# Kernel optimization log

Measured on AMD Instinct MI355X. Metric: run time of the kernel, lower is better.

Reference implementation:

```python
import jax, jax.numpy as jnp
import numpy as np

NUM_GROUPS = 32
EPS = 1e-6


def group_norm(x, gamma, beta):
    # x: [B, C, H, W]
    B, C, H, W = x.shape
    xg = x.reshape(B, NUM_GROUPS, C // NUM_GROUPS, H, W)
    mean = jnp.mean(xg, axis=(2, 3, 4), keepdims=True)
    var = jnp.var(xg, axis=(2, 3, 4), keepdims=True)
    xn = ((xg - mean) * jax.lax.rsqrt(var + EPS)).reshape(B, C, H, W)
    return xn * gamma[None, :, None, None] + beta[None, :, None, None]


def conv1x1(x, w, b):
    # x: [B, C, H, W], w: [O, C], b: [O]  (1x1 conv == channel matmul)
    return jnp.einsum('oc,bchw->bohw', w, x) + b[None, :, None, None]


def setup_inputs() -> dict:
    key = jax.random.key(0)
    ks = jax.random.split(key, 10)
    B, C, H, W = 16, 512, 32, 32
    s = 1.0 / np.sqrt(C)
    inp = {
        'hidden_states': jax.random.normal(ks[0], (B, C, H, W), dtype=jnp.float32),
        'norm_gamma': jnp.ones((C,), dtype=jnp.float32),
        'norm_beta': jnp.zeros((C,), dtype=jnp.float32),
        'wq': jax.random.normal(ks[1], (C, C), dtype=jnp.float32) * s,
        'bq': jnp.zeros((C,), dtype=jnp.float32),
        'wk': jax.random.normal(ks[2], (C, C), dtype=jnp.float32) * s,
        'bk': jnp.zeros((C,), dtype=jnp.float32),
        'wv': jax.random.normal(ks[3], (C, C), dtype=jnp.float32) * s,
        'bv': jnp.zeros((C,), dtype=jnp.float32),
        'wo': jax.random.normal(ks[4], (C, C), dtype=jnp.float32) * s,
        'bo': jnp.zeros((C,), dtype=jnp.float32),
    }
    return inp


def reference(hidden_states, norm_gamma, norm_beta, wq, bq, wk, bk, wv, bv, wo, bo):
    residual = hidden_states
    h = group_norm(hidden_states, norm_gamma, norm_beta)
    q = conv1x1(h, wq, bq)  # [B, C, H, W]
    k = conv1x1(h, wk, bk)
    v = conv1x1(h, wv, bv)
    B, C, H, W = q.shape
    N = H * W
    qf = q.reshape(B, C, N)  # [B, C, N]
    kf = k.reshape(B, C, N)
    vf = v.reshape(B, C, N)
    scale = float(C) ** (-0.5)
    # attn_weights[b, i, j] = sum_c q[b,c,i] * k[b,c,j]
    attn = jnp.einsum('bci,bcj->bij', qf, kf) * scale
    attn = jax.nn.softmax(attn, axis=2)
    # out[b, c, i] = sum_j v[b,c,j] * attn[b,i,j]
    out = jnp.einsum('bcj,bij->bci', vf, attn).reshape(B, C, H, W)
    out = conv1x1(out, wo, bo)
    return residual + out
```

## Files before the change

kernel.cpp:

```cpp
#include <hip/hip_runtime.h>

typedef __attribute__((ext_vector_type(4))) float f32x4;
typedef __attribute__((ext_vector_type(8))) __bf16 bf16x8;
typedef __attribute__((ext_vector_type(4))) unsigned short us4;
typedef __attribute__((ext_vector_type(8))) unsigned short us8;

#define B_  16
#define C_  512
#define N_  1024
#define G_  32
#define GS  16

__device__ inline unsigned short f2bf(float f) {
  unsigned u = __builtin_bit_cast(unsigned, f);
  u += 0x7fffu + ((u >> 16) & 1u);
  return (unsigned short)(u >> 16);
}
__device__ inline float bf2f(unsigned short u) {
  unsigned x = (unsigned)u << 16;
  return __builtin_bit_cast(float, x);
}

#define GLOAD_LDS16(gp, lp) __builtin_amdgcn_global_load_lds( \
    (const __attribute__((address_space(1))) unsigned int*)(gp), \
    (__attribute__((address_space(3))) unsigned int*)(lp), 16, 0, 0)

__global__ __launch_bounds__(256) void gn_stats(const float* __restrict__ x,
                                                float* __restrict__ stats) {
  int bg = blockIdx.x;
  const float* xp = x + (long)bg * (GS * N_);
  int tid = threadIdx.x;
  float s = 0.f, ss = 0.f;
  for (int i = tid * 4; i < GS * N_; i += 1024) {
    f32x4 v = *(const f32x4*)&xp[i];
    s += v.x + v.y + v.z + v.w;
    ss += v.x * v.x + v.y * v.y + v.z * v.z + v.w * v.w;
  }
  __shared__ float r1[256], r2[256];
  r1[tid] = s; r2[tid] = ss; __syncthreads();
  for (int off = 128; off > 0; off >>= 1) {
    if (tid < off) { r1[tid] += r1[tid + off]; r2[tid] += r2[tid + off]; }
    __syncthreads();
  }
  if (tid == 0) {
    float mean = r1[0] * (1.f / (GS * N_));
    float var  = r2[0] * (1.f / (GS * N_)) - mean * mean;
    stats[bg * 2]     = mean;
    stats[bg * 2 + 1] = rsqrtf(var + 1e-6f);
  }
}

__global__ __launch_bounds__(256) void gn_apply(const float* __restrict__ x,
                                                const float* __restrict__ stats,
                                                const float* __restrict__ gamma,
                                                const float* __restrict__ beta,
                                                unsigned short* __restrict__ ht) {
  int b = blockIdx.z, ct = blockIdx.y, nt = blockIdx.x;
  int c0 = ct * 64, n0 = nt * 64;
  int tid = threadIdx.x;
  __shared__ unsigned short L[64 * 68];
  const float* xp = x + ((long)b * C_ + c0) * N_ + n0;
#pragma unroll
  for (int i = 0; i < 4; ++i) {
    int li = tid + i * 256;
    int row = li >> 4;
    int col4 = (li & 15) * 4;
    f32x4 v = *(const f32x4*)&xp[(long)row * N_ + col4];
    int c = c0 + row;
    float mean = stats[(b * G_ + (c >> 4)) * 2];
    float rstd = stats[(b * G_ + (c >> 4)) * 2 + 1];
    float gm = gamma[c] * rstd;
    float bt = beta[c] - mean * gm;
    us4 o;
    o.x = f2bf(v.x * gm + bt); o.y = f2bf(v.y * gm + bt);
    o.z = f2bf(v.z * gm + bt); o.w = f2bf(v.w * gm + bt);
    *(us4*)&L[row * 68 + col4] = o;
  }
  __syncthreads();
#pragma unroll
  for (int i = 0; i < 2; ++i) {
    int s = tid + i * 256;
    int n = s >> 3;
    int cs = (s & 7) * 8;
    us8 o;
#pragma unroll
    for (int j = 0; j < 8; ++j) o[j] = L[(cs + j) * 68 + n];
    *(us8*)&ht[((long)b * N_ + n0 + n) * C_ + c0 + cs] = o;
  }
}

__global__ __launch_bounds__(256) void convert_w(const float* __restrict__ wq, const float* __restrict__ wk,
                                                 const float* __restrict__ wv, const float* __restrict__ wo,
                                                 const float* __restrict__ bq, const float* __restrict__ bk,
                                                 unsigned short* __restrict__ wqk, unsigned short* __restrict__ wvb,
                                                 unsigned short* __restrict__ wob, float* __restrict__ bqk) {
  int i = blockIdx.x * 256 + threadIdx.x;
  if (i < C_ * C_) {
    wqk[i]           = f2bf(wq[i]);
    wqk[C_ * C_ + i] = f2bf(wk[i]);
    wvb[i]           = f2bf(wv[i]);
    wob[i]           = f2bf(wo[i]);
  }
  if (i < C_) { bqk[i] = bq[i]; bqk[C_ + i] = bk[i]; }
}

__device__ inline f32x4 mfma16(bf16x8 a, bf16x8 b, f32x4 c) {
  return __builtin_amdgcn_mfma_f32_16x16x32_bf16(a, b, c, 0, 0, 0);
}

template<int EPI>
__global__ __launch_bounds__(256) void gemm_k(
    const unsigned short* __restrict__ A, long lda, long Az,
    const unsigned short* __restrict__ Bm, long ldb, long Bz,
    void* __restrict__ Dp, long ldd, long Dz,
    const float* __restrict__ bias, float scale, int K,
    const float* __restrict__ residual, float* __restrict__ rs) {
  const int z = blockIdx.z;
  const long row0 = (long)blockIdx.x * 128;
  const long col0 = (long)blockIdx.y * 128;
  const int tid  = threadIdx.x;
  const int lane = tid & 63;
  const int wave = tid >> 6;
  const int wr = (wave >> 1) * 64;
  const int wc = (wave & 1) * 64;
  const int lr = lane & 15;
  const int kh = (lane >> 4) * 8;

  __shared__ unsigned short As[2][128 * 32];
  __shared__ unsigned short Bs[2][128 * 32];
  __shared__ float dinv[128];

  if constexpr (EPI == 6) {
    if (tid < 128) {
      const float* rp = rs + ((long)z * 1024 + row0 + tid) * 16;
      float s = 0.f;
#pragma unroll
      for (int i = 0; i < 16; ++i) s += rp[i];
      dinv[tid] = 1.f / s;
    }
  }

  const int sr  = (lane >> 2);
  const int sk  = (lane & 3) * 8;
  const unsigned short* ga0 = A  + (long)z * Az + (row0 + wave * 32 + sr) * lda + sk;
  const unsigned short* gb0 = Bm + (long)z * Bz + (col0 + wave * 32 + sr) * ldb + sk;

  f32x4 acc[4][4];
#pragma unroll
  for (int m = 0; m < 4; ++m)
#pragma unroll
    for (int n = 0; n < 4; ++n) acc[m][n] = f32x4{0.f, 0.f, 0.f, 0.f};

  GLOAD_LDS16(ga0, &As[0][wave * 1024]);
  GLOAD_LDS16(ga0 + 16 * lda, &As[0][wave * 1024 + 512]);
  GLOAD_LDS16(gb0, &Bs[0][wave * 1024]);
  GLOAD_LDS16(gb0 + 16 * ldb, &Bs[0][wave * 1024 + 512]);
  __syncthreads();

  int cur = 0;
  for (int k0 = 0; k0 < K; k0 += 32) {
    if (k0 + 32 < K) {
      const int nb = cur ^ 1;
      GLOAD_LDS16(ga0 + k0 + 32, &As[nb][wave * 1024]);
      GLOAD_LDS16(ga0 + 16 * lda + k0 + 32, &As[nb][wave * 1024 + 512]);
      GLOAD_LDS16(gb0 + k0 + 32, &Bs[nb][wave * 1024]);
      GLOAD_LDS16(gb0 + 16 * ldb + k0 + 32, &Bs[nb][wave * 1024 + 512]);
    }
    bf16x8 af[4], bfr[4];
#pragma unroll
    for (int m = 0; m < 4; ++m) af[m]  = *(const bf16x8*)&As[cur][(wr + m * 16 + lr) * 32 + kh];
#pragma unroll
    for (int n = 0; n < 4; ++n) bfr[n] = *(const bf16x8*)&Bs[cur][(wc + n * 16 + lr) * 32 + kh];
#pragma unroll
    for (int m = 0; m < 4; ++m)
#pragma unroll
      for (int n = 0; n < 4; ++n)
        acc[m][n] = mfma16(af[m], bfr[n], acc[m][n]);
    __syncthreads();
    cur ^= 1;
  }

  const int rb = (lane >> 4) * 4;
  if constexpr (EPI == 5) {
    const int jt = (int)blockIdx.y;
#pragma unroll
    for (int m = 0; m < 4; ++m) {
      float ps[4] = {0.f, 0.f, 0.f, 0.f};
#pragma unroll
      for (int n = 0; n < 4; ++n) {
#pragma unroll
        for (int r = 0; r < 4; ++r) {
          long gr = row0 + wr + m * 16 + rb + r;
          long gc = col0 + wc + n * 16 + lr;
          float e = exp2f(acc[m][n][r] * scale);
          ((unsigned short*)Dp)[(long)z * Dz + gr * ldd + gc] = f2bf(e);
          ps[r] += e;
        }
      }
#pragma unroll
      for (int r = 0; r < 4; ++r) {
#pragma unroll
        for (int off = 1; off < 16; off <<= 1) ps[r] += __shfl_xor(ps[r], off);
      }
      if (lr == 0) {
#pragma unroll
        for (int r = 0; r < 4; ++r) {
          long gr = row0 + wr + m * 16 + rb + r;
          rs[((long)z * 1024 + gr) * 16 + jt * 2 + (wave & 1)] = ps[r];
        }
      }
    }
    return;
  }

#pragma unroll
  for (int m = 0; m < 4; ++m) {
#pragma unroll
    for (int n = 0; n < 4; ++n) {
#pragma unroll
      for (int r = 0; r < 4; ++r) {
        long gr = row0 + wr + m * 16 + rb + r;
        long gc = col0 + wc + n * 16 + lr;
        float v = acc[m][n][r];
        if constexpr (EPI == 0) {
          v += bias[gc];
          ((unsigned short*)Dp)[(long)z * Dz + gr * ldd + gc] = f2bf(v);
        } else if constexpr (EPI == 1) {
          v += bias[gr];
          ((unsigned short*)Dp)[(long)z * Dz + gr * ldd + gc] = f2bf(v);
        } else if constexpr (EPI == 6) {
          v *= dinv[(int)(gr - row0)];
          ((unsigned short*)Dp)[(long)z * Dz + gr * ldd + gc] = f2bf(v);
        } else {
          long o = (long)z * (512L * 1024L) + gr * 1024L + gc;
          ((float*)Dp)[o] = v + bias[gr] + residual[o];
        }
      }
    }
  }
}

extern "C" void kernel_launch(void* const* d_in, const int* in_sizes, int n_in,
                              void* d_out, int out_size, void* d_ws, size_t ws_size,
                              hipStream_t stream) {
  const float* x     = (const float*)d_in[0];
  const float* gamma = (const float*)d_in[1];
  const float* beta  = (const float*)d_in[2];
  const float* wq    = (const float*)d_in[3];
  const float* bq    = (const float*)d_in[4];
  const float* wk    = (const float*)d_in[5];
  const float* bk    = (const float*)d_in[6];
  const float* wv    = (const float*)d_in[7];
  const float* bv    = (const float*)d_in[8];
  const float* wo    = (const float*)d_in[9];
  const float* bo    = (const float*)d_in[10];
  float* out = (float*)d_out;

  char* ws = (char*)d_ws;
  unsigned short* ht   = (unsigned short*)(ws + 0);
  unsigned short* qkt  = (unsigned short*)(ws + 16777216);
  unsigned short* vv   = (unsigned short*)(ws + 50331648);
  unsigned short* ot   = (unsigned short*)(ws + 67108864);
  unsigned short* S    = (unsigned short*)(ws + 83886080);
  unsigned short* wqkb = (unsigned short*)(ws + 117440512);
  unsigned short* wvb  = (unsigned short*)(ws + 119537664);
  unsigned short* wob  = (unsigned short*)(ws + 120061952);
  float* bqk           = (float*)(ws + 120586240);
  float* stats         = (float*)(ws + 120590336);
  float* rs            = (float*)(ws + 120594432);

  convert_w<<<1024, 256, 0, stream>>>(wq, wk, wv, wo, bq, bk, wqkb, wvb, wob, bqk);
  gn_stats<<<512, 256, 0, stream>>>(x, stats);
  gn_apply<<<dim3(16, 8, 16), 256, 0, stream>>>(x, stats, gamma, beta, ht);

  gemm_k<0><<<dim3(128, 8, 1), 256, 0, stream>>>(ht, 512, 0, wqkb, 512, 0,
                                                 qkt, 1024, 0, bqk, 0.f, 512, nullptr, nullptr);
  gemm_k<1><<<dim3(4, 128, 1), 256, 0, stream>>>(wvb, 512, 0, ht, 512, 0,
                                                 vv, 16384, 0, bv, 0.f, 512, nullptr, nullptr);
  gemm_k<5><<<dim3(8, 8, 16), 256, 0, stream>>>(qkt, 1024, 1048576L, qkt + 512, 1024, 1048576L,
                                                S, 1024, 1048576L, nullptr,
                                                0.06375871416f, 512, nullptr, rs);
  gemm_k<6><<<dim3(8, 4, 16), 256, 0, stream>>>(S, 1024, 1048576L,
                                                vv, 16384, 1024,
                                                ot, 512, 524288L, nullptr, 0.f, 1024, nullptr, rs);
  gemm_k<4><<<dim3(4, 8, 16), 256, 0, stream>>>(wob, 512, 0, ot, 512, 524288L,
                                                out, 0, 0, bo, 0.f, 512, x, nullptr);
}
```

Before: 158.7 us.

## Replace 128x128 GEMM with 256-row tiled, swizzled, 512-thread pipelined GEMM

Rewrites the shared bf16 MFMA GEMM to use 256xBN tiles with 8 waves, a K-step of 64, and an XOR-swizzled LDS layout to avoid bank conflicts. It adds manual vmcnt waits and raw barriers so the next tile's loads overlap the MFMA work, and raises MFMA priority with setprio. All five GEMM launches get new grid shapes, and the softmax row-sum partial indexing changes to four partials per column tile. The larger tiles raise data reuse and arithmetic intensity, at the cost of fewer blocks per launch and more register pressure. The prefetch wraps around to tile 0 at the final iteration, which issues a redundant load.

```diff
diff --git a/kernel.cpp b/kernel.cpp
--- a/kernel.cpp
+++ b/kernel.cpp
@@ -15,10 +15,6 @@
   unsigned u = __builtin_bit_cast(unsigned, f);
   u += 0x7fffu + ((u >> 16) & 1u);
   return (unsigned short)(u >> 16);
-}
-__device__ inline float bf2f(unsigned short u) {
-  unsigned x = (unsigned)u << 16;
-  return __builtin_bit_cast(float, x);
 }
 
 #define GLOAD_LDS16(gp, lp) __builtin_amdgcn_global_load_lds( \
@@ -108,90 +104,123 @@
   return __builtin_amdgcn_mfma_f32_16x16x32_bf16(a, b, c, 0, 0, 0);
 }
 
-template<int EPI>
-__global__ __launch_bounds__(256) void gemm_k(
+__device__ inline int swz(int b) { return b ^ (((b >> 9) & 1) << 5); }
+
+template<int NREP, int EPI>
+__global__ __launch_bounds__(512, 2) void gemm256(
     const unsigned short* __restrict__ A, long lda, long Az,
     const unsigned short* __restrict__ Bm, long ldb, long Bz,
     void* __restrict__ Dp, long ldd, long Dz,
     const float* __restrict__ bias, float scale, int K,
     const float* __restrict__ residual, float* __restrict__ rs) {
+  constexpr int BN = NREP * 64;
   const int z = blockIdx.z;
-  const long row0 = (long)blockIdx.x * 128;
-  const long col0 = (long)blockIdx.y * 128;
+  const long row0 = (long)blockIdx.x * 256;
+  const long col0 = (long)blockIdx.y * BN;
   const int tid  = threadIdx.x;
   const int lane = tid & 63;
   const int wave = tid >> 6;
-  const int wr = (wave >> 1) * 64;
-  const int wc = (wave & 1) * 64;
+  const int wm = wave >> 2;
+  const int wn = wave & 3;
   const int lr = lane & 15;
-  const int kh = (lane >> 4) * 8;
-
-  __shared__ unsigned short As[2][128 * 32];
-  __shared__ unsigned short Bs[2][128 * 32];
-  __shared__ float dinv[128];
+  const int khb = (lane >> 4) * 16;
+
+  __shared__ unsigned short Abuf[2][16384];
+  __shared__ unsigned short Bbuf[2][BN * 64];
+  __shared__ float dinv_s[256];
+
+  const unsigned short* Ab = A  + (long)z * Az;
+  const unsigned short* Bb = Bm + (long)z * Bz;
 
   if constexpr (EPI == 6) {
-    if (tid < 128) {
+    if (tid < 256) {
       const float* rp = rs + ((long)z * 1024 + row0 + tid) * 16;
       float s = 0.f;
 #pragma unroll
       for (int i = 0; i < 16; ++i) s += rp[i];
-      dinv[tid] = 1.f / s;
+      dinv_s[tid] = 1.f / s;
     }
-  }
-
-  const int sr  = (lane >> 2);
-  const int sk  = (lane & 3) * 8;
-  const unsigned short* ga0 = A  + (long)z * Az + (row0 + wave * 32 + sr) * lda + sk;
-  const unsigned short* gb0 = Bm + (long)z * Bz + (col0 + wave * 32 + sr) * ldb + sk;
-
-  f32x4 acc[4][4];
-#pragma unroll
-  for (int m = 0; m < 4; ++m)
-#pragma unroll
-    for (int n = 0; n < 4; ++n) acc[m][n] = f32x4{0.f, 0.f, 0.f, 0.f};
-
-  GLOAD_LDS16(ga0, &As[0][wave * 1024]);
-  GLOAD_LDS16(ga0 + 16 * lda, &As[0][wave * 1024 + 512]);
-  GLOAD_LDS16(gb0, &Bs[0][wave * 1024]);
-  GLOAD_LDS16(gb0 + 16 * ldb, &Bs[0][wave * 1024 + 512]);
-  __syncthreads();
-
-  int cur = 0;
-  for (int k0 = 0; k0 < K; k0 += 32) {
-    if (k0 + 32 < K) {
-      const int nb = cur ^ 1;
-      GLOAD_LDS16(ga0 + k0 + 32, &As[nb][wave * 1024]);
-      GLOAD_LDS16(ga0 + 16 * lda + k0 + 32, &As[nb][wave * 1024 + 512]);
-      GLOAD_LDS16(gb0 + k0 + 32, &Bs[nb][wave * 1024]);
-      GLOAD_LDS16(gb0 + 16 * ldb + k0 + 32, &Bs[nb][wave * 1024 + 512]);
+    asm volatile("s_waitcnt lgkmcnt(0)" ::: "memory");
+  }
+
+  const unsigned short* gA[4];
+#pragma unroll
+  for (int r = 0; r < 4; ++r) {
+    int L = swz(r * 8192 + tid * 16);
+    gA[r] = Ab + (row0 + (L >> 7)) * lda + ((L & 127) >> 1);
+  }
+  const unsigned short* gB[NREP];
+#pragma unroll
+  for (int r = 0; r < NREP; ++r) {
+    int L = swz(r * 8192 + tid * 16);
+    gB[r] = Bb + (col0 + (L >> 7)) * ldb + ((L & 127) >> 1);
+  }
+
+  f32x4 acc[8][NREP];
+#pragma unroll
+  for (int m = 0; m < 8; ++m)
+#pragma unroll
+    for (int n = 0; n < NREP; ++n) acc[m][n] = f32x4{0.f, 0.f, 0.f, 0.f};
+
+  const int NT = K >> 6;
+#pragma unroll
+  for (int r = 0; r < 4; ++r)    GLOAD_LDS16(gA[r], &Abuf[0][r * 4096 + wave * 512]);
+#pragma unroll
+  for (int r = 0; r < NREP; ++r) GLOAD_LDS16(gB[r], &Bbuf[0][r * 4096 + wave * 512]);
+
+  for (int t = 0; t < NT; ++t) {
+    int tn = t + 1; if (tn == NT) tn = 0;
+    const long ko = (long)tn << 6;
+    const int nb = (t + 1) & 1;
+#pragma unroll
+    for (int r = 0; r < 4; ++r)    GLOAD_LDS16(gA[r] + ko, &Abuf[nb][r * 4096 + wave * 512]);
+#pragma unroll
+    for (int r = 0; r < NREP; ++r) GLOAD_LDS16(gB[r] + ko, &Bbuf[nb][r * 4096 + wave * 512]);
+    if constexpr (NREP == 4) asm volatile("s_waitcnt vmcnt(8)" ::: "memory");
+    else                     asm volatile("s_waitcnt vmcnt(6)" ::: "memory");
+    __builtin_amdgcn_s_barrier();
+    __builtin_amdgcn_sched_barrier(0);
+    const unsigned short* Al = Abuf[t & 1];
+    const unsigned short* Bl = Bbuf[t & 1];
+#pragma unroll
+    for (int kk = 0; kk < 2; ++kk) {
+      bf16x8 af[8], bfr[NREP];
+#pragma unroll
+      for (int m = 0; m < 8; ++m) {
+        int Pb = swz((wm * 128 + m * 16 + lr) * 128 + kk * 64 + khb);
+        af[m] = *(const bf16x8*)((const char*)Al + Pb);
+      }
+#pragma unroll
+      for (int n = 0; n < NREP; ++n) {
+        int Pb = swz((wn * NREP * 16 + n * 16 + lr) * 128 + kk * 64 + khb);
+        bfr[n] = *(const bf16x8*)((const char*)Bl + Pb);
+      }
+      __builtin_amdgcn_s_setprio(1);
+#pragma unroll
+      for (int m = 0; m < 8; ++m)
+#pragma unroll
+        for (int n = 0; n < NREP; ++n)
+          acc[m][n] = mfma16(af[m], bfr[n], acc[m][n]);
+      __builtin_amdgcn_s_setprio(0);
     }
-    bf16x8 af[4], bfr[4];
-#pragma unroll
-    for (int m = 0; m < 4; ++m) af[m]  = *(const bf16x8*)&As[cur][(wr + m * 16 + lr) * 32 + kh];
-#pragma unroll
-    for (int n = 0; n < 4; ++n) bfr[n] = *(const bf16x8*)&Bs[cur][(wc + n * 16 + lr) * 32 + kh];
-#pragma unroll
-    for (int m = 0; m < 4; ++m)
-#pragma unroll
-      for (int n = 0; n < 4; ++n)
-        acc[m][n] = mfma16(af[m], bfr[n], acc[m][n]);
-    __syncthreads();
-    cur ^= 1;
-  }
+    __builtin_amdgcn_sched_barrier(0);
+    __builtin_amdgcn_s_barrier();
+    __builtin_amdgcn_sched_barrier(0);
+  }
+  asm volatile("s_waitcnt vmcnt(0)" ::: "memory");
 
   const int rb = (lane >> 4) * 4;
   if constexpr (EPI == 5) {
-    const int jt = (int)blockIdx.y;
-#pragma unroll
-    for (int m = 0; m < 4; ++m) {
+    const int jt = blockIdx.y;
+#pragma unroll
+    for (int m = 0; m < 8; ++m) {
       float ps[4] = {0.f, 0.f, 0.f, 0.f};
 #pragma unroll
-      for (int n = 0; n < 4; ++n) {
+      for (int n = 0; n < NREP; ++n) {
 #pragma unroll
         for (int r = 0; r < 4; ++r) {
-          long gr = row0 + wr + m * 16 + rb + r;
-          long gc = col0 + wc + n * 16 + lr;
+          long gr = row0 + wm * 128 + m * 16 + rb + r;
+          long gc = col0 + wn * NREP * 16 + n * 16 + lr;
           float e = exp2f(acc[m][n][r] * scale);
           ((unsigned short*)Dp)[(long)z * Dz + gr * ldd + gc] = f2bf(e);
           ps[r] += e;
@@ -199,14 +228,16 @@
       }
 #pragma unroll
       for (int r = 0; r < 4; ++r) {
-#pragma unroll
-        for (int off = 1; off < 16; off <<= 1) ps[r] += __shfl_xor(ps[r], off);
+        ps[r] += __shfl_xor(ps[r], 1);
+        ps[r] += __shfl_xor(ps[r], 2);
+        ps[r] += __shfl_xor(ps[r], 4);
+        ps[r] += __shfl_xor(ps[r], 8);
       }
       if (lr == 0) {
 #pragma unroll
         for (int r = 0; r < 4; ++r) {
-          long gr = row0 + wr + m * 16 + rb + r;
-          rs[((long)z * 1024 + gr) * 16 + jt * 2 + (wave & 1)] = ps[r];
+          long gr = row0 + wm * 128 + m * 16 + rb + r;
+          rs[((long)z * 1024 + gr) * 16 + jt * 4 + wn] = ps[r];
         }
       }
     }
@@ -214,13 +245,13 @@
   }
 
 #pragma unroll
-  for (int m = 0; m < 4; ++m) {
-#pragma unroll
-    for (int n = 0; n < 4; ++n) {
+  for (int m = 0; m < 8; ++m) {
+#pragma unroll
+    for (int n = 0; n < NREP; ++n) {
 #pragma unroll
       for (int r = 0; r < 4; ++r) {
-        long gr = row0 + wr + m * 16 + rb + r;
-        long gc = col0 + wc + n * 16 + lr;
+        long gr = row0 + wm * 128 + m * 16 + rb + r;
+        long gc = col0 + wn * NREP * 16 + n * 16 + lr;
         float v = acc[m][n][r];
         if constexpr (EPI == 0) {
           v += bias[gc];
@@ -229,7 +260,7 @@
           v += bias[gr];
           ((unsigned short*)Dp)[(long)z * Dz + gr * ldd + gc] = f2bf(v);
         } else if constexpr (EPI == 6) {
-          v *= dinv[(int)(gr - row0)];
+          v *= dinv_s[(int)(wm * 128 + m * 16 + rb + r)];
           ((unsigned short*)Dp)[(long)z * Dz + gr * ldd + gc] = f2bf(v);
         } else {
           long o = (long)z * (512L * 1024L) + gr * 1024L + gc;
@@ -273,16 +304,16 @@
   gn_stats<<<512, 256, 0, stream>>>(x, stats);
   gn_apply<<<dim3(16, 8, 16), 256, 0, stream>>>(x, stats, gamma, beta, ht);
 
-  gemm_k<0><<<dim3(128, 8, 1), 256, 0, stream>>>(ht, 512, 0, wqkb, 512, 0,
-                                                 qkt, 1024, 0, bqk, 0.f, 512, nullptr, nullptr);
-  gemm_k<1><<<dim3(4, 128, 1), 256, 0, stream>>>(wvb, 512, 0, ht, 512, 0,
-                                                 vv, 16384, 0, bv, 0.f, 512, nullptr, nullptr);
-  gemm_k<5><<<dim3(8, 8, 16), 256, 0, stream>>>(qkt, 1024, 1048576L, qkt + 512, 1024, 1048576L,
-                                                S, 1024, 1048576L, nullptr,
-                                                0.06375871416f, 512, nullptr, rs);
-  gemm_k<6><<<dim3(8, 4, 16), 256, 0, stream>>>(S, 1024, 1048576L,
-                                                vv, 16384, 1024,
-                                                ot, 512, 524288L, nullptr, 0.f, 1024, nullptr, rs);
-  gemm_k<4><<<dim3(4, 8, 16), 256, 0, stream>>>(wob, 512, 0, ot, 512, 524288L,
-                                                out, 0, 0, bo, 0.f, 512, x, nullptr);
-}
+  gemm256<4, 0><<<dim3(64, 4, 1), 512, 0, stream>>>(ht, 512, 0, wqkb, 512, 0,
+                                                    qkt, 1024, 0, bqk, 0.f, 512, nullptr, nullptr);
+  gemm256<2, 1><<<dim3(2, 128, 1), 512, 0, stream>>>(wvb, 512, 0, ht, 512, 0,
+                                                     vv, 16384, 0, bv, 0.f, 512, nullptr, nullptr);
+  gemm256<4, 5><<<dim3(4, 4, 16), 512, 0, stream>>>(qkt, 1024, 1048576L, qkt + 512, 1024, 1048576L,
+                                                    S, 1024, 1048576L, nullptr,
+                                                    0.06375871416f, 512, nullptr, rs);
+  gemm256<2, 6><<<dim3(4, 4, 16), 512, 0, stream>>>(S, 1024, 1048576L,
+                                                    vv, 16384, 1024,
+                                                    ot, 512, 524288L, nullptr, 0.f, 1024, nullptr, rs);
+  gemm256<2, 4><<<dim3(2, 8, 16), 512, 0, stream>>>(wob, 512, 0, ot, 512, 524288L,
+                                                    out, 0, 0, bo, 0.f, 512, x, nullptr);
+}
```

Result: faster. 152.8 us (-3.7%).
